# Kernel tuning notes

Measured on AMD Instinct MI355X. Metric: run time of the kernel, lower is better.

## Reference

```python
import jax, jax.numpy as jnp
import numpy as np

N = 50000        # nodes
E = 800000       # edges
D = 64           # embedding_dim
N_GCN = 30       # stacked GCNConv layers
N_GGC = 8        # GatedGraphConv propagation steps


def setup_inputs() -> dict:
    key = jax.random.key(0)
    ks = jax.random.split(key, 12)
    s = 0.1
    x = jax.random.normal(ks[0], (N, 2 * D), dtype=jnp.float32)
    edge_index = jax.random.randint(ks[1], (2, E), 0, N, dtype=jnp.int32)
    return {
        "x": x,
        "edge_index": edge_index,
        "linear_w": jax.random.normal(ks[2], (D, 2 * D), dtype=jnp.float32) * s,
        "linear_b": jax.random.normal(ks[3], (D,), dtype=jnp.float32) * s,
        "gcn_w": jax.random.normal(ks[4], (N_GCN, D, D), dtype=jnp.float32) * s,
        "gcn_b": jax.random.normal(ks[5], (N_GCN, D), dtype=jnp.float32) * s,
        "ggc_w": jax.random.normal(ks[6], (N_GGC, D, D), dtype=jnp.float32) * s,
        "gru_w_ih": jax.random.normal(ks[7], (3 * D, D), dtype=jnp.float32) * s,
        "gru_w_hh": jax.random.normal(ks[8], (3 * D, D), dtype=jnp.float32) * s,
        "gru_b_ih": jax.random.normal(ks[9], (3 * D,), dtype=jnp.float32) * s,
        "gru_b_hh": jax.random.normal(ks[10], (3 * D,), dtype=jnp.float32) * s,
    }


def reference(x, edge_index, linear_w, linear_b, gcn_w, gcn_b,
              ggc_w, gru_w_ih, gru_w_hh, gru_b_ih, gru_b_hh):
    src, dst = edge_index[0], edge_index[1]

    # --- GCN normalization (self-loops added, symmetric deg^-1/2 norm) ---
    loop = jnp.arange(N, dtype=edge_index.dtype)
    src_sl = jnp.concatenate([src, loop])   # [E+N]
    dst_sl = jnp.concatenate([dst, loop])
    deg = jax.ops.segment_sum(jnp.ones(E + N, dtype=x.dtype), dst_sl, num_segments=N)
    dinv = deg ** -0.5                       # deg >= 1 because of self-loops
    norm = (dinv[src_sl] * dinv[dst_sl])[:, None]  # [E+N, 1]

    # --- initial linear + relu ---
    h = jax.nn.relu(x @ linear_w.T + linear_b)      # [N, D]

    # --- 30 stacked GCNConv layers (NOTE: original's in-loop relu is a no-op) ---
    def gcn_step(h, wb):
        W, b = wb
        xw = h @ W.T                                 # [N, D]
        msg = xw[src_sl] * norm                      # [E+N, D] gather
        out = jax.ops.segment_sum(msg, dst_sl, num_segments=N) + b
        return out, None

    h, _ = jax.lax.scan(gcn_step, h, (gcn_w, gcn_b))

    # --- GatedGraphConv(D, num_layers=8): add-aggregation + GRUCell ---
    def ggc_step(h, W):
        m = jax.ops.segment_sum((h @ W)[src], dst, num_segments=N)  # [N, D]
        gi = m @ gru_w_ih.T + gru_b_ih              # [N, 3D]
        gh = h @ gru_w_hh.T + gru_b_hh
        ir, iz, inn = jnp.split(gi, 3, axis=1)
        hr, hz, hn = jnp.split(gh, 3, axis=1)
        r = jax.nn.sigmoid(ir + hr)
        z = jax.nn.sigmoid(iz + hz)
        n = jnp.tanh(inn + r * hn)
        h_new = (1.0 - z) * n + z * h
        return h_new, None

    h, _ = jax.lax.scan(ggc_step, h, ggc_w)
    # l2 / gate / cross_graph in the original are dead code; only h is returned
    return h
```

## Files before the change

kernel.cpp:

```cpp
#include <hip/hip_runtime.h>
#include <math.h>

#define NN 50000
#define NE 800000
#define DD 64
#define N_GCN 30
#define N_GGC 8
#define NB ((NN + 255) / 256)

__device__ __forceinline__ float lane_bcast(float v, int k) {
    return __int_as_float(__builtin_amdgcn_readlane(__float_as_int(v), k));
}


__global__ void hist_kernel(const int* __restrict__ dst, int* __restrict__ cnt) {
    int i = blockIdx.x * blockDim.x + threadIdx.x;
    if (i < NE) atomicAdd(&cnt[dst[i]], 1);
}

__global__ void dinv_kernel(const int* __restrict__ cnt, float* __restrict__ dinv) {
    int i = blockIdx.x * blockDim.x + threadIdx.x;
    if (i < NN) dinv[i] = rsqrtf((float)cnt[i] + 1.0f);
}

__global__ void scan1_kernel(const int* __restrict__ cnt, int* __restrict__ bsum) {
    __shared__ int s[256];
    int tid = threadIdx.x;
    int i = blockIdx.x * 256 + tid;
    s[tid] = (i < NN) ? cnt[i] : 0;
    __syncthreads();
    for (int off = 128; off > 0; off >>= 1) {
        if (tid < off) s[tid] += s[tid + off];
        __syncthreads();
    }
    if (tid == 0) bsum[blockIdx.x] = s[0];
}

__global__ void scan2_kernel(int* __restrict__ bsum) {
    if (threadIdx.x == 0 && blockIdx.x == 0) {
        int acc = 0;
        for (int b = 0; b < NB; b++) { int v = bsum[b]; bsum[b] = acc; acc += v; }
        bsum[NB] = acc;
    }
}

__global__ void scan3_kernel(const int* __restrict__ cnt, const int* __restrict__ bsum,
                             int* __restrict__ rowptr) {
    __shared__ int s[256];
    int tid = threadIdx.x;
    int i = blockIdx.x * 256 + tid;
    int v = (i < NN) ? cnt[i] : 0;
    s[tid] = v;
    __syncthreads();
    for (int off = 1; off < 256; off <<= 1) {
        int t = (tid >= off) ? s[tid - off] : 0;
        __syncthreads();
        s[tid] += t;
        __syncthreads();
    }
    if (i < NN) rowptr[i] = bsum[blockIdx.x] + s[tid] - v;
    if (i == NN - 1) rowptr[NN] = bsum[blockIdx.x] + s[tid];
}

__global__ void fill_kernel(const int* __restrict__ src, const int* __restrict__ dst,
                            const float* __restrict__ dinv, const int* __restrict__ rowptr,
                            int* __restrict__ cur, int2* __restrict__ epk) {
    int i = blockIdx.x * blockDim.x + threadIdx.x;
    if (i >= NE) return;
    int s = src[i], d = dst[i];
    int pos = atomicAdd(&cur[d], 1);
    int idx = rowptr[d] + pos;
    float w = dinv[s] * dinv[d];
    epk[idx] = make_int2(s, __float_as_int(w));
}


__global__ void prep_weights(const float* __restrict__ lw, const float* __restrict__ gw,
                             const float* __restrict__ wih, const float* __restrict__ whh,
                             float* __restrict__ lin_wt, float* __restrict__ gcn_wt,
                             float* __restrict__ wih_t, float* __restrict__ whh_t) {
    int i = blockIdx.x * blockDim.x + threadIdx.x;
    if (i < 8192) {
        int k = i >> 6, j = i & 63;
        lin_wt[k * 64 + j] = lw[j * 128 + k];
    }
    if (i < 122880) {
        int l = i >> 12, r = i & 4095;
        int k = r >> 6, j = r & 63;
        gcn_wt[l * 4096 + k * 64 + j] = gw[l * 4096 + j * 64 + k];
    }
    if (i < 12288) {
        int j = i >> 6, k = i & 63;
        wih_t[k * 192 + j] = wih[i];
        whh_t[k * 192 + j] = whh[i];
    }
}


__global__ __launch_bounds__(256) void init_linear(const float* __restrict__ x,
                                                   const float* __restrict__ lin_wt,
                                                   const float* __restrict__ lb,
                                                   float* __restrict__ h) {
    int lane = threadIdx.x & 63;
    int wv = blockIdx.x * (blockDim.x >> 6) + (threadIdx.x >> 6);
    int nw = gridDim.x * (blockDim.x >> 6);
    float w[128];
#pragma unroll
    for (int k = 0; k < 128; k++) w[k] = lin_wt[k * 64 + lane];
    float b = lb[lane];
    for (int n = wv; n < NN; n += nw) {
        float x0 = x[n * 128 + lane];
        float x1 = x[n * 128 + 64 + lane];
        float a0 = b, a1 = 0.f, a2 = 0.f, a3 = 0.f;
#pragma unroll
        for (int k = 0; k < 64; k += 4) {
            a0 = fmaf(lane_bcast(x0, k), w[k], a0);
            a1 = fmaf(lane_bcast(x0, k + 1), w[k + 1], a1);
            a2 = fmaf(lane_bcast(x0, k + 2), w[k + 2], a2);
            a3 = fmaf(lane_bcast(x0, k + 3), w[k + 3], a3);
        }
#pragma unroll
        for (int k = 0; k < 64; k += 4) {
            a0 = fmaf(lane_bcast(x1, k), w[64 + k], a0);
            a1 = fmaf(lane_bcast(x1, k + 1), w[64 + k + 1], a1);
            a2 = fmaf(lane_bcast(x1, k + 2), w[64 + k + 2], a2);
            a3 = fmaf(lane_bcast(x1, k + 3), w[64 + k + 3], a3);
        }
        h[n * 64 + lane] = fmaxf((a0 + a1) + (a2 + a3), 0.0f);
    }
}


__global__ __launch_bounds__(256) void mm64_kernel(const float* __restrict__ in,
                                                   const float* __restrict__ wt,
                                                   float* __restrict__ out) {
    int lane = threadIdx.x & 63;
    int wv = blockIdx.x * (blockDim.x >> 6) + (threadIdx.x >> 6);
    int nw = gridDim.x * (blockDim.x >> 6);
    float w[64];
#pragma unroll
    for (int k = 0; k < 64; k++) w[k] = wt[k * 64 + lane];
    for (int n = wv; n < NN; n += nw) {
        float hreg = in[n * 64 + lane];
        float a0 = 0.f, a1 = 0.f, a2 = 0.f, a3 = 0.f;
#pragma unroll
        for (int k = 0; k < 64; k += 4) {
            a0 = fmaf(lane_bcast(hreg, k), w[k], a0);
            a1 = fmaf(lane_bcast(hreg, k + 1), w[k + 1], a1);
            a2 = fmaf(lane_bcast(hreg, k + 2), w[k + 2], a2);
            a3 = fmaf(lane_bcast(hreg, k + 3), w[k + 3], a3);
        }
        out[n * 64 + lane] = (a0 + a1) + (a2 + a3);
    }
}


__global__ __launch_bounds__(256, 2) void mm192_kernel(const float* __restrict__ in,
                                                       const float* __restrict__ wt,
                                                       const float* __restrict__ bias,
                                                       float* __restrict__ out) {
    int lane = threadIdx.x & 63;
    int wv = blockIdx.x * (blockDim.x >> 6) + (threadIdx.x >> 6);
    int nw = gridDim.x * (blockDim.x >> 6);
    float w[192];
#pragma unroll
    for (int k = 0; k < 64; k++) {
        w[k * 3 + 0] = wt[k * 192 + lane];
        w[k * 3 + 1] = wt[k * 192 + 64 + lane];
        w[k * 3 + 2] = wt[k * 192 + 128 + lane];
    }
    float b0 = bias[lane], b1 = bias[64 + lane], b2 = bias[128 + lane];
    for (int n = wv; n < NN; n += nw) {
        float hreg = in[n * 64 + lane];
        float a0 = b0, a1 = b1, a2 = b2;
#pragma unroll
        for (int k = 0; k < 64; k++) {
            float hv = lane_bcast(hreg, k);
            a0 = fmaf(hv, w[k * 3 + 0], a0);
            a1 = fmaf(hv, w[k * 3 + 1], a1);
            a2 = fmaf(hv, w[k * 3 + 2], a2);
        }
        out[n * 192 + lane] = a0;
        out[n * 192 + 64 + lane] = a1;
        out[n * 192 + 128 + lane] = a2;
    }
}


template <bool NORM>
__global__ __launch_bounds__(256) void agg_kernel(const float* __restrict__ xw,
                                                  const int* __restrict__ rowptr,
                                                  const int2* __restrict__ epk,
                                                  const float* __restrict__ dinv,
                                                  const float* __restrict__ bias,
                                                  float* __restrict__ out) {
    int lane = threadIdx.x & 63;
    int sub = lane >> 4;
    int q = lane & 15;
    int wv = blockIdx.x * (blockDim.x >> 6) + (threadIdx.x >> 6);
    int nw = gridDim.x * (blockDim.x >> 6);

    float4 b4 = make_float4(0.f, 0.f, 0.f, 0.f);
    if (NORM) b4 = *(const float4*)&bias[q * 4];

    for (int n = wv; n < NN; n += nw) {
        int e0 = rowptr[n], e1 = rowptr[n + 1];
        float ax = 0.f, ay = 0.f, az = 0.f, aw = 0.f;

        int e = e0 + sub;
        while (e + 4 < e1) {
            int2 p0 = epk[e];
            int2 p1 = epk[e + 4];
            float4 v0 = *(const float4*)&xw[(size_t)p0.x * 64 + q * 4];
            float4 v1 = *(const float4*)&xw[(size_t)p1.x * 64 + q * 4];
            float w0 = NORM ? __int_as_float(p0.y) : 1.0f;
            float w1 = NORM ? __int_as_float(p1.y) : 1.0f;
            ax = fmaf(w0, v0.x, ax); ay = fmaf(w0, v0.y, ay);
            az = fmaf(w0, v0.z, az); aw = fmaf(w0, v0.w, aw);
            ax = fmaf(w1, v1.x, ax); ay = fmaf(w1, v1.y, ay);
            az = fmaf(w1, v1.z, az); aw = fmaf(w1, v1.w, aw);
            e += 8;
        }
        if (e < e1) {
            int2 p0 = epk[e];
            float4 v0 = *(const float4*)&xw[(size_t)p0.x * 64 + q * 4];
            float w0 = NORM ? __int_as_float(p0.y) : 1.0f;
            ax = fmaf(w0, v0.x, ax); ay = fmaf(w0, v0.y, ay);
            az = fmaf(w0, v0.z, az); aw = fmaf(w0, v0.w, aw);
        }

        ax += __shfl_xor(ax, 16); ay += __shfl_xor(ay, 16);
        az += __shfl_xor(az, 16); aw += __shfl_xor(aw, 16);
        ax += __shfl_xor(ax, 32); ay += __shfl_xor(ay, 32);
        az += __shfl_xor(az, 32); aw += __shfl_xor(aw, 32);

        if (sub == 0) {
            float4 r;
            if (NORM) {
                float di = dinv[n];
                float dd = di * di;
                float4 sv = *(const float4*)&xw[(size_t)n * 64 + q * 4];
                r.x = ax + b4.x + dd * sv.x;
                r.y = ay + b4.y + dd * sv.y;
                r.z = az + b4.z + dd * sv.z;
                r.w = aw + b4.w + dd * sv.w;
            } else {
                r.x = ax; r.y = ay; r.z = az; r.w = aw;
            }
            *(float4*)&out[(size_t)n * 64 + q * 4] = r;
        }
    }
}


__global__ __launch_bounds__(256, 2) void gru_kernel(const float* __restrict__ hin,
                                                     const float* __restrict__ gi,
                                                     const float* __restrict__ whh_t,
                                                     const float* __restrict__ bhh,
                                                     float* __restrict__ hout) {
    int lane = threadIdx.x & 63;
    int wv = blockIdx.x * (blockDim.x >> 6) + (threadIdx.x >> 6);
    int nw = gridDim.x * (blockDim.x >> 6);
    float w[192];
#pragma unroll
    for (int k = 0; k < 64; k++) {
        w[k * 3 + 0] = whh_t[k * 192 + lane];
        w[k * 3 + 1] = whh_t[k * 192 + 64 + lane];
        w[k * 3 + 2] = whh_t[k * 192 + 128 + lane];
    }
    float b0 = bhh[lane], b1 = bhh[64 + lane], b2 = bhh[128 + lane];
    for (int n = wv; n < NN; n += nw) {
        float hreg = hin[n * 64 + lane];
        float a0 = b0, a1 = b1, a2 = b2;
#pragma unroll
        for (int k = 0; k < 64; k++) {
            float hv = lane_bcast(hreg, k);
            a0 = fmaf(hv, w[k * 3 + 0], a0);
            a1 = fmaf(hv, w[k * 3 + 1], a1);
            a2 = fmaf(hv, w[k * 3 + 2], a2);
        }
        float ir = gi[n * 192 + lane];
        float iz = gi[n * 192 + 64 + lane];
        float in_ = gi[n * 192 + 128 + lane];
        float r = 1.0f / (1.0f + expf(-(ir + a0)));
        float z = 1.0f / (1.0f + expf(-(iz + a1)));
        float nn = tanhf(in_ + r * a2);
        hout[n * 64 + lane] = (1.0f - z) * nn + z * hreg;
    }
}


extern "C" void kernel_launch(void* const* d_in, const int* in_sizes, int n_in,
                              void* d_out, int out_size, void* d_ws, size_t ws_size,
                              hipStream_t stream) {
    const float* x   = (const float*)d_in[0];
    const int*   ei  = (const int*)d_in[1];
    const int*   src = ei;
    const int*   dst = ei + NE;
    const float* lw  = (const float*)d_in[2];
    const float* lb  = (const float*)d_in[3];
    const float* gw  = (const float*)d_in[4];
    const float* gb  = (const float*)d_in[5];
    const float* ggw = (const float*)d_in[6];
    const float* wih = (const float*)d_in[7];
    const float* whh = (const float*)d_in[8];
    const float* bih = (const float*)d_in[9];
    const float* bhh = (const float*)d_in[10];
    float* outp = (float*)d_out;

    char* ws = (char*)d_ws;
    size_t off = 0;
    auto take = [&](size_t bytes) -> char* {
        char* p = ws + off;
        off += (bytes + 255) & ~(size_t)255;
        return p;
    };
    int*   cnt    = (int*)take(NN * 4);
    int*   cur    = (int*)take(NN * 4);
    int*   rowptr = (int*)take((NN + 1) * 4);
    int*   bsum   = (int*)take((NB + 1) * 4);
    float* dinv   = (float*)take(NN * 4);
    int2*  epk    = (int2*)take((size_t)NE * 8);
    float* lin_wt = (float*)take(8192 * 4);
    float* gcn_wt = (float*)take(122880 * 4);
    float* wih_t  = (float*)take(12288 * 4);
    float* whh_t  = (float*)take(12288 * 4);
    float* h      = (float*)take((size_t)NN * 64 * 4);
    float* t0     = (float*)take((size_t)NN * 64 * 4);
    float* t1     = (float*)take((size_t)NN * 64 * 4);
    float* gi     = (float*)take((size_t)NN * 192 * 4);
    (void)ws_size; (void)in_sizes; (void)n_in; (void)out_size;

    hipMemsetAsync(cnt, 0, NN * 4, stream);
    hipMemsetAsync(cur, 0, NN * 4, stream);

    hist_kernel<<<(NE + 255) / 256, 256, 0, stream>>>(dst, cnt);
    dinv_kernel<<<(NN + 255) / 256, 256, 0, stream>>>(cnt, dinv);
    scan1_kernel<<<NB, 256, 0, stream>>>(cnt, bsum);
    scan2_kernel<<<1, 64, 0, stream>>>(bsum);
    scan3_kernel<<<NB, 256, 0, stream>>>(cnt, bsum, rowptr);
    fill_kernel<<<(NE + 255) / 256, 256, 0, stream>>>(src, dst, dinv, rowptr, cur, epk);
    prep_weights<<<480, 256, 0, stream>>>(lw, gw, wih, whh, lin_wt, gcn_wt, wih_t, whh_t);

    init_linear<<<512, 256, 0, stream>>>(x, lin_wt, lb, h);

    for (int l = 0; l < N_GCN; l++) {
        mm64_kernel<<<1024, 256, 0, stream>>>(h, gcn_wt + l * 4096, t0);
        agg_kernel<true><<<(NN + 3) / 4, 256, 0, stream>>>(t0, rowptr, epk, dinv,
                                                           gb + l * 64, h);
    }

    for (int l = 0; l < N_GGC; l++) {
        mm64_kernel<<<1024, 256, 0, stream>>>(h, ggw + l * 4096, t0);
        agg_kernel<false><<<(NN + 3) / 4, 256, 0, stream>>>(t0, rowptr, epk, nullptr,
                                                            nullptr, t1);
        mm192_kernel<<<512, 256, 0, stream>>>(t1, wih_t, bih, gi);
        float* hdst = (l == N_GGC - 1) ? outp : h;
        gru_kernel<<<512, 256, 0, stream>>>(h, gi, whh_t, bhh, hdst);
    }
}
```

Before: 2.552 ms.

## Fuse GCN/GGC weight matmul into aggregation and split GRU into gate matmul plus elementwise

Uses linearity to aggregate neighbour features first and then apply the 64x64 weight inside the aggregation kernel, removing the separate mm64 pass and its intermediate buffer for every GCN and GGC layer. GCN layers now ping-pong between two buffers. The GRU stage is restructured: a gate_mm kernel computes both input and hidden gate projections one 64-wide chunk per wave into new gi/gh buffers, and a separate elementwise kernel applies the GRU nonlinearity. In exchange, every wave reloads its weight slice per node (one node per wave), and gh adds an extra large buffer round-trip through memory.

```diff
diff --git a/kernel.cpp b/kernel.cpp
--- a/kernel.cpp
+++ b/kernel.cpp
@@ -131,77 +131,23 @@
 }
 
 
-__global__ __launch_bounds__(256) void mm64_kernel(const float* __restrict__ in,
-                                                   const float* __restrict__ wt,
-                                                   float* __restrict__ out) {
-    int lane = threadIdx.x & 63;
-    int wv = blockIdx.x * (blockDim.x >> 6) + (threadIdx.x >> 6);
-    int nw = gridDim.x * (blockDim.x >> 6);
-    float w[64];
-#pragma unroll
-    for (int k = 0; k < 64; k++) w[k] = wt[k * 64 + lane];
-    for (int n = wv; n < NN; n += nw) {
-        float hreg = in[n * 64 + lane];
-        float a0 = 0.f, a1 = 0.f, a2 = 0.f, a3 = 0.f;
-#pragma unroll
-        for (int k = 0; k < 64; k += 4) {
-            a0 = fmaf(lane_bcast(hreg, k), w[k], a0);
-            a1 = fmaf(lane_bcast(hreg, k + 1), w[k + 1], a1);
-            a2 = fmaf(lane_bcast(hreg, k + 2), w[k + 2], a2);
-            a3 = fmaf(lane_bcast(hreg, k + 3), w[k + 3], a3);
-        }
-        out[n * 64 + lane] = (a0 + a1) + (a2 + a3);
-    }
-}
-
-
-__global__ __launch_bounds__(256, 2) void mm192_kernel(const float* __restrict__ in,
-                                                       const float* __restrict__ wt,
-                                                       const float* __restrict__ bias,
-                                                       float* __restrict__ out) {
-    int lane = threadIdx.x & 63;
-    int wv = blockIdx.x * (blockDim.x >> 6) + (threadIdx.x >> 6);
-    int nw = gridDim.x * (blockDim.x >> 6);
-    float w[192];
-#pragma unroll
-    for (int k = 0; k < 64; k++) {
-        w[k * 3 + 0] = wt[k * 192 + lane];
-        w[k * 3 + 1] = wt[k * 192 + 64 + lane];
-        w[k * 3 + 2] = wt[k * 192 + 128 + lane];
-    }
-    float b0 = bias[lane], b1 = bias[64 + lane], b2 = bias[128 + lane];
-    for (int n = wv; n < NN; n += nw) {
-        float hreg = in[n * 64 + lane];
-        float a0 = b0, a1 = b1, a2 = b2;
-#pragma unroll
-        for (int k = 0; k < 64; k++) {
-            float hv = lane_bcast(hreg, k);
-            a0 = fmaf(hv, w[k * 3 + 0], a0);
-            a1 = fmaf(hv, w[k * 3 + 1], a1);
-            a2 = fmaf(hv, w[k * 3 + 2], a2);
-        }
-        out[n * 192 + lane] = a0;
-        out[n * 192 + 64 + lane] = a1;
-        out[n * 192 + 128 + lane] = a2;
-    }
-}
-
-
 template <bool NORM>
-__global__ __launch_bounds__(256) void agg_kernel(const float* __restrict__ xw,
-                                                  const int* __restrict__ rowptr,
-                                                  const int2* __restrict__ epk,
-                                                  const float* __restrict__ dinv,
-                                                  const float* __restrict__ bias,
-                                                  float* __restrict__ out) {
+__global__ __launch_bounds__(256) void agg_fused(const float* __restrict__ hin,
+                                                 const int* __restrict__ rowptr,
+                                                 const int2* __restrict__ epk,
+                                                 const float* __restrict__ dinv,
+                                                 const float* __restrict__ wt,
+                                                 const float* __restrict__ bias,
+                                                 float* __restrict__ out) {
     int lane = threadIdx.x & 63;
     int sub = lane >> 4;
     int q = lane & 15;
     int wv = blockIdx.x * (blockDim.x >> 6) + (threadIdx.x >> 6);
     int nw = gridDim.x * (blockDim.x >> 6);
 
-    float4 b4 = make_float4(0.f, 0.f, 0.f, 0.f);
-    if (NORM) b4 = *(const float4*)&bias[q * 4];
+    float w[64];
+#pragma unroll
+    for (int k = 0; k < 64; k++) w[k] = wt[k * 64 + lane];
 
     for (int n = wv; n < NN; n += nw) {
         int e0 = rowptr[n], e1 = rowptr[n + 1];
@@ -211,8 +157,8 @@
         while (e + 4 < e1) {
             int2 p0 = epk[e];
             int2 p1 = epk[e + 4];
-            float4 v0 = *(const float4*)&xw[(size_t)p0.x * 64 + q * 4];
-            float4 v1 = *(const float4*)&xw[(size_t)p1.x * 64 + q * 4];
+            float4 v0 = *(const float4*)&hin[(size_t)p0.x * 64 + q * 4];
+            float4 v1 = *(const float4*)&hin[(size_t)p1.x * 64 + q * 4];
             float w0 = NORM ? __int_as_float(p0.y) : 1.0f;
             float w1 = NORM ? __int_as_float(p1.y) : 1.0f;
             ax = fmaf(w0, v0.x, ax); ay = fmaf(w0, v0.y, ay);
@@ -223,7 +169,7 @@
         }
         if (e < e1) {
             int2 p0 = epk[e];
-            float4 v0 = *(const float4*)&xw[(size_t)p0.x * 64 + q * 4];
+            float4 v0 = *(const float4*)&hin[(size_t)p0.x * 64 + q * 4];
             float w0 = NORM ? __int_as_float(p0.y) : 1.0f;
             ax = fmaf(w0, v0.x, ax); ay = fmaf(w0, v0.y, ay);
             az = fmaf(w0, v0.z, az); aw = fmaf(w0, v0.w, aw);
@@ -234,59 +180,98 @@
         ax += __shfl_xor(ax, 32); ay += __shfl_xor(ay, 32);
         az += __shfl_xor(az, 32); aw += __shfl_xor(aw, 32);
 
-        if (sub == 0) {
-            float4 r;
-            if (NORM) {
-                float di = dinv[n];
-                float dd = di * di;
-                float4 sv = *(const float4*)&xw[(size_t)n * 64 + q * 4];
-                r.x = ax + b4.x + dd * sv.x;
-                r.y = ay + b4.y + dd * sv.y;
-                r.z = az + b4.z + dd * sv.z;
-                r.w = aw + b4.w + dd * sv.w;
-            } else {
-                r.x = ax; r.y = ay; r.z = az; r.w = aw;
-            }
-            *(float4*)&out[(size_t)n * 64 + q * 4] = r;
-        }
-    }
-}
-
-
-__global__ __launch_bounds__(256, 2) void gru_kernel(const float* __restrict__ hin,
-                                                     const float* __restrict__ gi,
-                                                     const float* __restrict__ whh_t,
-                                                     const float* __restrict__ bhh,
-                                                     float* __restrict__ hout) {
+        if (NORM) {
+            float di = dinv[n];
+            float dd = di * di;
+            float4 sv = *(const float4*)&hin[(size_t)n * 64 + q * 4];
+            ax = fmaf(dd, sv.x, ax); ay = fmaf(dd, sv.y, ay);
+            az = fmaf(dd, sv.z, az); aw = fmaf(dd, sv.w, aw);
+        }
+
+        float acc0 = NORM ? bias[lane] : 0.0f;
+        float acc1 = 0.f;
+#pragma unroll
+        for (int k = 0; k < 64; k += 4) {
+            acc0 = fmaf(lane_bcast(ax, k >> 2), w[k], acc0);
+            acc1 = fmaf(lane_bcast(ay, k >> 2), w[k + 1], acc1);
+            acc0 = fmaf(lane_bcast(az, k >> 2), w[k + 2], acc0);
+            acc1 = fmaf(lane_bcast(aw, k >> 2), w[k + 3], acc1);
+        }
+        out[(size_t)n * 64 + lane] = acc0 + acc1;
+    }
+}
+
+
+__global__ __launch_bounds__(256) void gate_mm(const float* __restrict__ t1,
+                                               const float* __restrict__ h,
+                                               const float* __restrict__ wih_t,
+                                               const float* __restrict__ whh_t,
+                                               const float* __restrict__ bih,
+                                               const float* __restrict__ bhh,
+                                               float* __restrict__ gi,
+                                               float* __restrict__ gh) {
     int lane = threadIdx.x & 63;
     int wv = blockIdx.x * (blockDim.x >> 6) + (threadIdx.x >> 6);
-    int nw = gridDim.x * (blockDim.x >> 6);
-    float w[192];
-#pragma unroll
-    for (int k = 0; k < 64; k++) {
-        w[k * 3 + 0] = whh_t[k * 192 + lane];
-        w[k * 3 + 1] = whh_t[k * 192 + 64 + lane];
-        w[k * 3 + 2] = whh_t[k * 192 + 128 + lane];
-    }
-    float b0 = bhh[lane], b1 = bhh[64 + lane], b2 = bhh[128 + lane];
-    for (int n = wv; n < NN; n += nw) {
-        float hreg = hin[n * 64 + lane];
-        float a0 = b0, a1 = b1, a2 = b2;
+    int nt = gridDim.x * (blockDim.x >> 6);
+    for (int t = wv; t < NN * 3; t += nt) {
+        int c = t / NN;
+        int n = t - c * NN;
+        float wi[64], wh[64];
 #pragma unroll
         for (int k = 0; k < 64; k++) {
-            float hv = lane_bcast(hreg, k);
-            a0 = fmaf(hv, w[k * 3 + 0], a0);
-            a1 = fmaf(hv, w[k * 3 + 1], a1);
-            a2 = fmaf(hv, w[k * 3 + 2], a2);
-        }
-        float ir = gi[n * 192 + lane];
-        float iz = gi[n * 192 + 64 + lane];
-        float in_ = gi[n * 192 + 128 + lane];
-        float r = 1.0f / (1.0f + expf(-(ir + a0)));
-        float z = 1.0f / (1.0f + expf(-(iz + a1)));
-        float nn = tanhf(in_ + r * a2);
-        hout[n * 64 + lane] = (1.0f - z) * nn + z * hreg;
-    }
+            wi[k] = wih_t[k * 192 + c * 64 + lane];
+            wh[k] = whh_t[k * 192 + c * 64 + lane];
+        }
+        float tv = t1[(size_t)n * 64 + lane];
+        float hv = h[(size_t)n * 64 + lane];
+        float ai = bih[c * 64 + lane];
+        float ah = bhh[c * 64 + lane];
+#pragma unroll
+        for (int k = 0; k < 64; k++) {
+            float b1 = lane_bcast(tv, k);
+            float b2 = lane_bcast(hv, k);
+            ai = fmaf(b1, wi[k], ai);
+            ah = fmaf(b2, wh[k], ah);
+        }
+        gi[(size_t)n * 192 + c * 64 + lane] = ai;
+        gh[(size_t)n * 192 + c * 64 + lane] = ah;
+    }
+}
+
+
+__global__ __launch_bounds__(256) void gru_elem(const float* __restrict__ gi,
+                                                const float* __restrict__ gh,
+                                                const float* __restrict__ h,
+                                                float* __restrict__ hout) {
+    int i = blockIdx.x * blockDim.x + threadIdx.x;
+    if (i >= NN * 16) return;
+    int n = i >> 4, q = i & 15;
+    size_t base = (size_t)n * 192 + q * 4;
+    float4 ir = *(const float4*)&gi[base];
+    float4 iz = *(const float4*)&gi[base + 64];
+    float4 in_ = *(const float4*)&gi[base + 128];
+    float4 hr = *(const float4*)&gh[base];
+    float4 hz = *(const float4*)&gh[base + 64];
+    float4 hn = *(const float4*)&gh[base + 128];
+    float4 hv = *(const float4*)&h[(size_t)n * 64 + q * 4];
+    float4 r, z, nn, o;
+    r.x = 1.f / (1.f + expf(-(ir.x + hr.x)));
+    r.y = 1.f / (1.f + expf(-(ir.y + hr.y)));
+    r.z = 1.f / (1.f + expf(-(ir.z + hr.z)));
+    r.w = 1.f / (1.f + expf(-(ir.w + hr.w)));
+    z.x = 1.f / (1.f + expf(-(iz.x + hz.x)));
+    z.y = 1.f / (1.f + expf(-(iz.y + hz.y)));
+    z.z = 1.f / (1.f + expf(-(iz.z + hz.z)));
+    z.w = 1.f / (1.f + expf(-(iz.w + hz.w)));
+    nn.x = tanhf(in_.x + r.x * hn.x);
+    nn.y = tanhf(in_.y + r.y * hn.y);
+    nn.z = tanhf(in_.z + r.z * hn.z);
+    nn.w = tanhf(in_.w + r.w * hn.w);
+    o.x = (1.f - z.x) * nn.x + z.x * hv.x;
+    o.y = (1.f - z.y) * nn.y + z.y * hv.y;
+    o.z = (1.f - z.z) * nn.z + z.z * hv.z;
+    o.w = (1.f - z.w) * nn.w + z.w * hv.w;
+    *(float4*)&hout[(size_t)n * 64 + q * 4] = o;
 }
 
 
@@ -329,6 +314,7 @@
     float* t0     = (float*)take((size_t)NN * 64 * 4);
     float* t1     = (float*)take((size_t)NN * 64 * 4);
     float* gi     = (float*)take((size_t)NN * 192 * 4);
+    float* gh     = (float*)take((size_t)NN * 192 * 4);
     (void)ws_size; (void)in_sizes; (void)n_in; (void)out_size;
 
     hipMemsetAsync(cnt, 0, NN * 4, stream);
@@ -344,18 +330,19 @@
 
     init_linear<<<512, 256, 0, stream>>>(x, lin_wt, lb, h);
 
+    float* cur_h = h;
+    float* nxt_h = t0;
     for (int l = 0; l < N_GCN; l++) {
-        mm64_kernel<<<1024, 256, 0, stream>>>(h, gcn_wt + l * 4096, t0);
-        agg_kernel<true><<<(NN + 3) / 4, 256, 0, stream>>>(t0, rowptr, epk, dinv,
-                                                           gb + l * 64, h);
+        agg_fused<true><<<(NN + 3) / 4, 256, 0, stream>>>(cur_h, rowptr, epk, dinv,
+                                                          gcn_wt + l * 4096, gb + l * 64, nxt_h);
+        float* tmp = cur_h; cur_h = nxt_h; nxt_h = tmp;
     }
 
     for (int l = 0; l < N_GGC; l++) {
-        mm64_kernel<<<1024, 256, 0, stream>>>(h, ggw + l * 4096, t0);
-        agg_kernel<false><<<(NN + 3) / 4, 256, 0, stream>>>(t0, rowptr, epk, nullptr,
-                                                            nullptr, t1);
-        mm192_kernel<<<512, 256, 0, stream>>>(t1, wih_t, bih, gi);
-        float* hdst = (l == N_GGC - 1) ? outp : h;
-        gru_kernel<<<512, 256, 0, stream>>>(h, gi, whh_t, bhh, hdst);
-    }
-}
+        agg_fused<false><<<(NN + 3) / 4, 256, 0, stream>>>(cur_h, rowptr, epk, nullptr,
+                                                           ggw + l * 4096, nullptr, t1);
+        gate_mm<<<37500, 256, 0, stream>>>(t1, cur_h, wih_t, whh_t, bih, bhh, gi, gh);
+        float* hdst = (l == N_GGC - 1) ? outp : cur_h;
+        gru_elem<<<(NN * 16 + 255) / 256, 256, 0, stream>>>(gi, gh, cur_h, hdst);
+    }
+}
```

Measured after the change: 3.703 ms. 45.1% more time.

## Aggregate before transform and fold GGC weights into GRU input matrices

Applied to the files above, without the earlier changes.

GCN layers now aggregate raw features first and apply the weight matrix plus bias afterwards, using linearity (A·H·W = (A·H)·W). For GatedGraphConv, each step's propagation weight is pre-multiplied into the GRU input weights on the device, so aggregation reads h directly. The separate m and gi projections and the GRU kernel are merged into one 384-thread kernel that stages six gate outputs per node in LDS. The intermediate gi buffer disappears and there are fewer launches, in exchange for __syncthreads per node batch, fast-math exp/tanh approximations and a small change in floating-point rounding order.

```diff
diff --git a/kernel.cpp b/kernel.cpp
--- a/kernel.cpp
+++ b/kernel.cpp
@@ -7,6 +7,7 @@
 #define N_GCN 30
 #define N_GGC 8
 #define NB ((NN + 255) / 256)
+#define NPB 6
 
 __device__ __forceinline__ float lane_bcast(float v, int k) {
     return __int_as_float(__builtin_amdgcn_readlane(__float_as_int(v), k));
@@ -97,6 +98,43 @@
 }
 
 
+__global__ void prep_comb(const float* __restrict__ ggw, const float* __restrict__ wih_t,
+                          const float* __restrict__ whh_t, const float* __restrict__ bih,
+                          const float* __restrict__ bhh,
+                          float* __restrict__ WB, float* __restrict__ BB) {
+    int tid = blockIdx.x * blockDim.x + threadIdx.x;
+    int wv = tid >> 6, lane = tid & 63;
+    if (wv < 24) {
+        int l = wv / 3, c = wv - l * 3;
+        float u[64];
+#pragma unroll
+        for (int m = 0; m < 64; m++) u[m] = wih_t[m * 192 + c * 64 + lane];
+        for (int k = 0; k < 64; k++) {
+            float v = ggw[l * 4096 + k * 64 + lane];
+            float a0 = 0.f, a1 = 0.f, a2 = 0.f, a3 = 0.f;
+#pragma unroll
+            for (int m = 0; m < 64; m += 4) {
+                a0 = fmaf(lane_bcast(v, m), u[m], a0);
+                a1 = fmaf(lane_bcast(v, m + 1), u[m + 1], a1);
+                a2 = fmaf(lane_bcast(v, m + 2), u[m + 2], a2);
+                a3 = fmaf(lane_bcast(v, m + 3), u[m + 3], a3);
+            }
+            WB[l * 24576 + c * 4096 + k * 64 + lane] = (a0 + a1) + (a2 + a3);
+        }
+    }
+    int nthr = blockDim.x * gridDim.x;
+    for (int idx = tid; idx < 98304; idx += nthr) {
+        int l = idx / 12288;
+        int rem = idx - l * 12288;
+        int c = rem >> 12;
+        int r2 = rem & 4095;
+        int k = r2 >> 6, j = r2 & 63;
+        WB[l * 24576 + (3 + c) * 4096 + k * 64 + j] = whh_t[k * 192 + c * 64 + j];
+    }
+    if (tid < 384) BB[tid] = (tid < 192) ? bih[tid] : bhh[tid - 192];
+}
+
+
 __global__ __launch_bounds__(256) void init_linear(const float* __restrict__ x,
                                                    const float* __restrict__ lin_wt,
                                                    const float* __restrict__ lb,
@@ -131,78 +169,18 @@
 }
 
 
-__global__ __launch_bounds__(256) void mm64_kernel(const float* __restrict__ in,
-                                                   const float* __restrict__ wt,
-                                                   float* __restrict__ out) {
-    int lane = threadIdx.x & 63;
-    int wv = blockIdx.x * (blockDim.x >> 6) + (threadIdx.x >> 6);
-    int nw = gridDim.x * (blockDim.x >> 6);
-    float w[64];
-#pragma unroll
-    for (int k = 0; k < 64; k++) w[k] = wt[k * 64 + lane];
-    for (int n = wv; n < NN; n += nw) {
-        float hreg = in[n * 64 + lane];
-        float a0 = 0.f, a1 = 0.f, a2 = 0.f, a3 = 0.f;
-#pragma unroll
-        for (int k = 0; k < 64; k += 4) {
-            a0 = fmaf(lane_bcast(hreg, k), w[k], a0);
-            a1 = fmaf(lane_bcast(hreg, k + 1), w[k + 1], a1);
-            a2 = fmaf(lane_bcast(hreg, k + 2), w[k + 2], a2);
-            a3 = fmaf(lane_bcast(hreg, k + 3), w[k + 3], a3);
-        }
-        out[n * 64 + lane] = (a0 + a1) + (a2 + a3);
-    }
-}
-
-
-__global__ __launch_bounds__(256, 2) void mm192_kernel(const float* __restrict__ in,
-                                                       const float* __restrict__ wt,
-                                                       const float* __restrict__ bias,
-                                                       float* __restrict__ out) {
-    int lane = threadIdx.x & 63;
-    int wv = blockIdx.x * (blockDim.x >> 6) + (threadIdx.x >> 6);
-    int nw = gridDim.x * (blockDim.x >> 6);
-    float w[192];
-#pragma unroll
-    for (int k = 0; k < 64; k++) {
-        w[k * 3 + 0] = wt[k * 192 + lane];
-        w[k * 3 + 1] = wt[k * 192 + 64 + lane];
-        w[k * 3 + 2] = wt[k * 192 + 128 + lane];
-    }
-    float b0 = bias[lane], b1 = bias[64 + lane], b2 = bias[128 + lane];
-    for (int n = wv; n < NN; n += nw) {
-        float hreg = in[n * 64 + lane];
-        float a0 = b0, a1 = b1, a2 = b2;
-#pragma unroll
-        for (int k = 0; k < 64; k++) {
-            float hv = lane_bcast(hreg, k);
-            a0 = fmaf(hv, w[k * 3 + 0], a0);
-            a1 = fmaf(hv, w[k * 3 + 1], a1);
-            a2 = fmaf(hv, w[k * 3 + 2], a2);
-        }
-        out[n * 192 + lane] = a0;
-        out[n * 192 + 64 + lane] = a1;
-        out[n * 192 + 128 + lane] = a2;
-    }
-}
-
-
 template <bool NORM>
-__global__ __launch_bounds__(256) void agg_kernel(const float* __restrict__ xw,
-                                                  const int* __restrict__ rowptr,
-                                                  const int2* __restrict__ epk,
-                                                  const float* __restrict__ dinv,
-                                                  const float* __restrict__ bias,
-                                                  float* __restrict__ out) {
+__global__ __launch_bounds__(256) void agg_raw(const float* __restrict__ hin,
+                                               const int* __restrict__ rowptr,
+                                               const int2* __restrict__ epk,
+                                               const float* __restrict__ dinv,
+                                               float* __restrict__ out) {
     int lane = threadIdx.x & 63;
     int sub = lane >> 4;
     int q = lane & 15;
     int wv = blockIdx.x * (blockDim.x >> 6) + (threadIdx.x >> 6);
     int nw = gridDim.x * (blockDim.x >> 6);
 
-    float4 b4 = make_float4(0.f, 0.f, 0.f, 0.f);
-    if (NORM) b4 = *(const float4*)&bias[q * 4];
-
     for (int n = wv; n < NN; n += nw) {
         int e0 = rowptr[n], e1 = rowptr[n + 1];
         float ax = 0.f, ay = 0.f, az = 0.f, aw = 0.f;
@@ -211,8 +189,8 @@
         while (e + 4 < e1) {
             int2 p0 = epk[e];
             int2 p1 = epk[e + 4];
-            float4 v0 = *(const float4*)&xw[(size_t)p0.x * 64 + q * 4];
-            float4 v1 = *(const float4*)&xw[(size_t)p1.x * 64 + q * 4];
+            float4 v0 = *(const float4*)&hin[(size_t)p0.x * 64 + q * 4];
+            float4 v1 = *(const float4*)&hin[(size_t)p1.x * 64 + q * 4];
             float w0 = NORM ? __int_as_float(p0.y) : 1.0f;
             float w1 = NORM ? __int_as_float(p1.y) : 1.0f;
             ax = fmaf(w0, v0.x, ax); ay = fmaf(w0, v0.y, ay);
@@ -223,7 +201,7 @@
         }
         if (e < e1) {
             int2 p0 = epk[e];
-            float4 v0 = *(const float4*)&xw[(size_t)p0.x * 64 + q * 4];
+            float4 v0 = *(const float4*)&hin[(size_t)p0.x * 64 + q * 4];
             float w0 = NORM ? __int_as_float(p0.y) : 1.0f;
             ax = fmaf(w0, v0.x, ax); ay = fmaf(w0, v0.y, ay);
             az = fmaf(w0, v0.z, az); aw = fmaf(w0, v0.w, aw);
@@ -239,11 +217,11 @@
             if (NORM) {
                 float di = dinv[n];
                 float dd = di * di;
-                float4 sv = *(const float4*)&xw[(size_t)n * 64 + q * 4];
-                r.x = ax + b4.x + dd * sv.x;
-                r.y = ay + b4.y + dd * sv.y;
-                r.z = az + b4.z + dd * sv.z;
-                r.w = aw + b4.w + dd * sv.w;
+                float4 sv = *(const float4*)&hin[(size_t)n * 64 + q * 4];
+                r.x = fmaf(dd, sv.x, ax);
+                r.y = fmaf(dd, sv.y, ay);
+                r.z = fmaf(dd, sv.z, az);
+                r.w = fmaf(dd, sv.w, aw);
             } else {
                 r.x = ax; r.y = ay; r.z = az; r.w = aw;
             }
@@ -253,39 +231,81 @@
 }
 
 
-__global__ __launch_bounds__(256, 2) void gru_kernel(const float* __restrict__ hin,
-                                                     const float* __restrict__ gi,
-                                                     const float* __restrict__ whh_t,
-                                                     const float* __restrict__ bhh,
-                                                     float* __restrict__ hout) {
+__global__ __launch_bounds__(256) void mm64b(const float* __restrict__ in,
+                                             const float* __restrict__ wt,
+                                             const float* __restrict__ bias,
+                                             float* __restrict__ out) {
     int lane = threadIdx.x & 63;
     int wv = blockIdx.x * (blockDim.x >> 6) + (threadIdx.x >> 6);
     int nw = gridDim.x * (blockDim.x >> 6);
-    float w[192];
-#pragma unroll
-    for (int k = 0; k < 64; k++) {
-        w[k * 3 + 0] = whh_t[k * 192 + lane];
-        w[k * 3 + 1] = whh_t[k * 192 + 64 + lane];
-        w[k * 3 + 2] = whh_t[k * 192 + 128 + lane];
-    }
-    float b0 = bhh[lane], b1 = bhh[64 + lane], b2 = bhh[128 + lane];
+    float w[64];
+#pragma unroll
+    for (int k = 0; k < 64; k++) w[k] = wt[k * 64 + lane];
+    float b = bias[lane];
     for (int n = wv; n < NN; n += nw) {
-        float hreg = hin[n * 64 + lane];
-        float a0 = b0, a1 = b1, a2 = b2;
-#pragma unroll
-        for (int k = 0; k < 64; k++) {
-            float hv = lane_bcast(hreg, k);
-            a0 = fmaf(hv, w[k * 3 + 0], a0);
-            a1 = fmaf(hv, w[k * 3 + 1], a1);
-            a2 = fmaf(hv, w[k * 3 + 2], a2);
-        }
-        float ir = gi[n * 192 + lane];
-        float iz = gi[n * 192 + 64 + lane];
-        float in_ = gi[n * 192 + 128 + lane];
-        float r = 1.0f / (1.0f + expf(-(ir + a0)));
-        float z = 1.0f / (1.0f + expf(-(iz + a1)));
-        float nn = tanhf(in_ + r * a2);
-        hout[n * 64 + lane] = (1.0f - z) * nn + z * hreg;
+        float hreg = in[(size_t)n * 64 + lane];
+        float a0 = b, a1 = 0.f, a2 = 0.f, a3 = 0.f;
+#pragma unroll
+        for (int k = 0; k < 64; k += 4) {
+            a0 = fmaf(lane_bcast(hreg, k), w[k], a0);
+            a1 = fmaf(lane_bcast(hreg, k + 1), w[k + 1], a1);
+            a2 = fmaf(lane_bcast(hreg, k + 2), w[k + 2], a2);
+            a3 = fmaf(lane_bcast(hreg, k + 3), w[k + 3], a3);
+        }
+        out[(size_t)n * 64 + lane] = (a0 + a1) + (a2 + a3);
+    }
+}
+
+
+__global__ __launch_bounds__(384) void gru_fused(const float* __restrict__ t1,
+                                                 const float* __restrict__ h,
+                                                 const float* __restrict__ WBl,
+                                                 const float* __restrict__ BB,
+                                                 float* __restrict__ hout) {
+    __shared__ float lds[NPB * 384];
+    int tid = threadIdx.x;
+    int g = tid >> 6, lane = tid & 63;
+    const float* wptr = WBl + (g << 12);
+    float w[64];
+#pragma unroll
+    for (int k = 0; k < 64; k++) w[k] = wptr[k * 64 + lane];
+    float bb = BB[g * 64 + lane];
+    const float* in = (g < 3) ? t1 : h;
+
+    for (int base = blockIdx.x * NPB; base < NN; base += gridDim.x * NPB) {
+        for (int i = 0; i < NPB; i++) {
+            int n = base + i;
+            if (n < NN) {
+                float v = in[(size_t)n * 64 + lane];
+                float a0 = bb, a1 = 0.f, a2 = 0.f, a3 = 0.f;
+#pragma unroll
+                for (int k = 0; k < 64; k += 4) {
+                    a0 = fmaf(lane_bcast(v, k), w[k], a0);
+                    a1 = fmaf(lane_bcast(v, k + 1), w[k + 1], a1);
+                    a2 = fmaf(lane_bcast(v, k + 2), w[k + 2], a2);
+                    a3 = fmaf(lane_bcast(v, k + 3), w[k + 3], a3);
+                }
+                lds[i * 384 + g * 64 + lane] = (a0 + a1) + (a2 + a3);
+            }
+        }
+        __syncthreads();
+        int n2 = base + g;
+        if (n2 < NN) {
+            float ir = lds[g * 384 + lane];
+            float iz = lds[g * 384 + 64 + lane];
+            float inn = lds[g * 384 + 128 + lane];
+            float hr = lds[g * 384 + 192 + lane];
+            float hz = lds[g * 384 + 256 + lane];
+            float hn = lds[g * 384 + 320 + lane];
+            float hv = h[(size_t)n2 * 64 + lane];
+            float r = 1.0f / (1.0f + __expf(-(ir + hr)));
+            float z = 1.0f / (1.0f + __expf(-(iz + hz)));
+            float targ = inn + r * hn;
+            float t2 = __expf(2.0f * targ);
+            float nn2 = 1.0f - 2.0f / (t2 + 1.0f);
+            hout[(size_t)n2 * 64 + lane] = (1.0f - z) * nn2 + z * hv;
+        }
+        __syncthreads();
     }
 }
 
@@ -325,10 +345,10 @@
     float* gcn_wt = (float*)take(122880 * 4);
     float* wih_t  = (float*)take(12288 * 4);
     float* whh_t  = (float*)take(12288 * 4);
+    float* WB     = (float*)take(196608 * 4);
+    float* BB     = (float*)take(384 * 4);
     float* h      = (float*)take((size_t)NN * 64 * 4);
-    float* t0     = (float*)take((size_t)NN * 64 * 4);
     float* t1     = (float*)take((size_t)NN * 64 * 4);
-    float* gi     = (float*)take((size_t)NN * 192 * 4);
     (void)ws_size; (void)in_sizes; (void)n_in; (void)out_size;
 
     hipMemsetAsync(cnt, 0, NN * 4, stream);
@@ -341,21 +361,18 @@
     scan3_kernel<<<NB, 256, 0, stream>>>(cnt, bsum, rowptr);
     fill_kernel<<<(NE + 255) / 256, 256, 0, stream>>>(src, dst, dinv, rowptr, cur, epk);
     prep_weights<<<480, 256, 0, stream>>>(lw, gw, wih, whh, lin_wt, gcn_wt, wih_t, whh_t);
+    prep_comb<<<96, 256, 0, stream>>>(ggw, wih_t, whh_t, bih, bhh, WB, BB);
 
     init_linear<<<512, 256, 0, stream>>>(x, lin_wt, lb, h);
 
     for (int l = 0; l < N_GCN; l++) {
-        mm64_kernel<<<1024, 256, 0, stream>>>(h, gcn_wt + l * 4096, t0);
-        agg_kernel<true><<<(NN + 3) / 4, 256, 0, stream>>>(t0, rowptr, epk, dinv,
-                                                           gb + l * 64, h);
+        agg_raw<true><<<12500, 256, 0, stream>>>(h, rowptr, epk, dinv, t1);
+        mm64b<<<1024, 256, 0, stream>>>(t1, gcn_wt + l * 4096, gb + l * 64, h);
     }
 
     for (int l = 0; l < N_GGC; l++) {
-        mm64_kernel<<<1024, 256, 0, stream>>>(h, ggw + l * 4096, t0);
-        agg_kernel<false><<<(NN + 3) / 4, 256, 0, stream>>>(t0, rowptr, epk, nullptr,
-                                                            nullptr, t1);
-        mm192_kernel<<<512, 256, 0, stream>>>(t1, wih_t, bih, gi);
+        agg_raw<false><<<12500, 256, 0, stream>>>(h, rowptr, epk, nullptr, t1);
         float* hdst = (l == N_GGC - 1) ? outp : h;
-        gru_kernel<<<512, 256, 0, stream>>>(h, gi, whh_t, bhh, hdst);
-    }
-}
+        gru_fused<<<1024, 384, 0, stream>>>(t1, h, WB + l * 24576, BB, hdst);
+    }
+}
```

Result: no change. 2.594 ms (+1.6%).
